# Optimization experiments

Hardware: AMD Instinct MI355X
Metric: run time of the kernel (lower is better)

## Reference

```python
import jax, jax.numpy as jnp
import numpy as np

B, T, C = 4, 2048, 1024
H = 16
D = C // H  # head_dim = 64


def setup_inputs() -> dict:
    key = jax.random.key(0)
    ks = jax.random.split(key, 9)
    s = 1.0 / np.sqrt(C)
    return {
        "x": jax.random.normal(ks[0], (B, T, C), dtype=jnp.float32),
        "Wk": jax.random.uniform(ks[1], (C, C), jnp.float32, -s, s),
        "bk": jax.random.uniform(ks[2], (C,), jnp.float32, -s, s),
        "Wq": jax.random.uniform(ks[3], (C, C), jnp.float32, -s, s),
        "bq": jax.random.uniform(ks[4], (C,), jnp.float32, -s, s),
        "Wv": jax.random.uniform(ks[5], (C, C), jnp.float32, -s, s),
        "bv": jax.random.uniform(ks[6], (C,), jnp.float32, -s, s),
        "Wp": jax.random.uniform(ks[7], (C, C), jnp.float32, -s, s),
        "bp": jax.random.uniform(ks[8], (C,), jnp.float32, -s, s),
    }


def reference(x, Wk, bk, Wq, bq, Wv, bv, Wp, bp):
    # projections -> (B, H, T, D)
    def split_heads(y):
        return y.reshape(B, T, H, D).transpose(0, 2, 1, 3)

    k = split_heads(x @ Wk.T + bk)
    q = split_heads(x @ Wq.T + bq)
    v = split_heads(x @ Wv.T + bv)

    att = jnp.einsum("bhtd,bhsd->bhts", q, k) / np.sqrt(D).astype(np.float32)
    causal = jnp.tril(jnp.ones((T, T), dtype=bool))
    att = jnp.where(causal, att, -jnp.inf)
    att = jax.nn.softmax(att, axis=-1)

    y = jnp.einsum("bhts,bhsd->bhtd", att, v)  # (B,H,T,D)
    y = y.transpose(0, 2, 1, 3).reshape(B, T, C)
    return y @ Wp.T + bp
```

## Files before the change

kernel.cpp:

```cpp
#include <hip/hip_runtime.h>
#include <hip/hip_bf16.h>

typedef unsigned short u16;
typedef unsigned int u32;
typedef short short8 __attribute__((ext_vector_type(8)));
typedef short short4v __attribute__((ext_vector_type(4)));
typedef float f32x4 __attribute__((ext_vector_type(4)));

#define MFMA16(a, b, c) __builtin_amdgcn_mfma_f32_16x16x32_bf16((a), (b), (c), 0, 0, 0)

constexpr int kB = 4, kT = 2048, kC = 1024, kH = 16, kD = 64;
constexpr int kBT = kB * kT;
constexpr long kQKV = (long)kB * kH * kT * kD;
constexpr float kSC = 0.125f * 1.4426950408889634f;

__device__ inline u16 f2bf(float f) {
    __hip_bfloat16 h = __float2bfloat16(f);
    return *reinterpret_cast<u16*>(&h);
}
__device__ inline u32 pkbf_trunc(float lo, float hi) {
    return __builtin_amdgcn_perm(__builtin_bit_cast(u32, hi),
                                 __builtin_bit_cast(u32, lo), 0x07060302u);
}
__device__ inline u32 pkbf_rne(float lo, float hi) {
    return ((u32)f2bf(hi) << 16) | (u32)f2bf(lo);
}

__device__ inline void cp16(const u16* g, u16* l) {
    __builtin_amdgcn_global_load_lds(
        (const __attribute__((address_space(1))) unsigned int*)g,
        (__attribute__((address_space(3))) unsigned int*)l, 16, 0, 0);
}

__global__ __launch_bounds__(256) void cast_kernel(
    const float* __restrict__ x,  const float* __restrict__ Wk,
    const float* __restrict__ Wq, const float* __restrict__ Wv,
    const float* __restrict__ Wp,
    u16* __restrict__ xb, u16* __restrict__ wkb, u16* __restrict__ wqb,
    u16* __restrict__ wvb, u16* __restrict__ wpb)
{
    const long id = (long)blockIdx.x * 256 + threadIdx.x;
    const float* src;
    u16* dst;
    long off;
    if (id < 2097152) {
        src = x; dst = xb; off = id;
    } else {
        const long w = (id - 2097152) >> 18;
        off = (id - 2097152) & 262143;
        src = (w == 0) ? Wk : (w == 1) ? Wq : (w == 2) ? Wv : Wp;
        dst = (w == 0) ? wkb : (w == 1) ? wqb : (w == 2) ? wvb : wpb;
    }
    f32x4 v = *(const f32x4*)&src[off * 4];
    short4v s = {(short)f2bf(v[0]), (short)f2bf(v[1]),
                 (short)f2bf(v[2]), (short)f2bf(v[3])};
    *(short4v*)&dst[off * 4] = s;
}


__global__ __launch_bounds__(512, 1) void qkv_gemm_bf16(
    const u16* __restrict__ xb, const u16* __restrict__ wall,
    const float* __restrict__ bk, const float* __restrict__ bq,
    const float* __restrict__ bv,
    u16* __restrict__ kw, u16* __restrict__ qw, u16* __restrict__ vw)
{
    __shared__ __align__(16) u16 A2[2][128 * 64];
    __shared__ __align__(16) u16 B2[2][256 * 64];

    const int tid = threadIdx.x;
    const int lane = tid & 63;
    const int wid = tid >> 6;
    const int l15 = lane & 15;
    const int quad = lane >> 4;
    const int wr = wid & 1;
    const int wc = wid >> 1;
    const int m0 = blockIdx.x * 128;
    const int n0c = blockIdx.y * 256;

    f32x4 zero = {0.f, 0.f, 0.f, 0.f};
    f32x4 acc[4][4];
#pragma unroll
    for (int i = 0; i < 4; ++i)
#pragma unroll
        for (int j = 0; j < 4; ++j) acc[i][j] = zero;

    const int vA = tid >> 3, chA = tid & 7;
    const int rowMa = ((vA >> 5) << 6) + (vA & 31);
    const int rowMb = rowMa + 32;
    const u16* aMaS = xb + (long)(m0 + rowMa) * kC + ((chA ^ (rowMa & 7)) * 8);
    const u16* aMbS = xb + (long)(m0 + rowMb) * kC + ((chA ^ (rowMb & 7)) * 8);
    const int aMaD = rowMa * 64 + chA * 8;
    const int aMbD = rowMb * 64 + chA * 8;
    const u16* bNaS[2]; const u16* bNbS[2];
    int bNaD[2], bNbD[2];
#pragma unroll
    for (int q = 0; q < 2; ++q) {
        const int slot = q * 512 + tid;
        const int v = slot >> 3, ch = slot & 7;
        const int ra = ((v >> 5) << 6) + (v & 31);
        const int rb = ra + 32;
        bNaS[q] = wall + (long)(n0c + ra) * kC + ((ch ^ (ra & 7)) * 8);
        bNbS[q] = wall + (long)(n0c + rb) * kC + ((ch ^ (rb & 7)) * 8);
        bNaD[q] = ra * 64 + ch * 8;
        bNbD[q] = rb * 64 + ch * 8;
    }

    int aOff[4][2], bOff[4][2];
#pragma unroll
    for (int i = 0; i < 4; ++i) {
        const int row = wr * 64 + i * 16 + l15;
#pragma unroll
        for (int k2 = 0; k2 < 2; ++k2)
            aOff[i][k2] = row * 64 + (((k2 * 4 + quad) ^ (row & 7)) * 8);
    }
#pragma unroll
    for (int j = 0; j < 4; ++j) {
        const int row = wc * 64 + j * 16 + l15;
#pragma unroll
        for (int k2 = 0; k2 < 2; ++k2)
            bOff[j][k2] = row * 64 + (((k2 * 4 + quad) ^ (row & 7)) * 8);
    }

    cp16(bNaS[0], &B2[0][bNaD[0]]);
    cp16(bNaS[1], &B2[0][bNaD[1]]);
    cp16(aMaS,    &A2[0][aMaD]);
    cp16(aMbS,    &A2[0][aMbD]);
    cp16(bNbS[0], &B2[0][bNbD[0]]);
    cp16(bNbS[1], &B2[0][bNbD[1]]);

#pragma unroll 2
    for (int t = 0; t < 16; ++t) {
        const int c = t & 1;
        const u16* Ab = A2[c];
        const u16* Bb = B2[c];
        u16* An = A2[c ^ 1];
        u16* Bn = B2[c ^ 1];
        const long ko = (long)(t + 1) * 64;
        const bool pf = (t < 15);

        short8 amL[2][2], amH[2][2], bnL[2][2], bnH[2][2];

        asm volatile("s_waitcnt vmcnt(2)" ::: "memory");
        __builtin_amdgcn_s_barrier();
        __builtin_amdgcn_sched_barrier(0);
#pragma unroll
        for (int i = 0; i < 2; ++i)
#pragma unroll
            for (int k2 = 0; k2 < 2; ++k2)
                amL[i][k2] = *(const short8*)&Ab[aOff[i][k2]];
#pragma unroll
        for (int j = 0; j < 2; ++j)
#pragma unroll
            for (int k2 = 0; k2 < 2; ++k2)
                bnL[j][k2] = *(const short8*)&Bb[bOff[j][k2]];
        if (pf) {
            cp16(bNaS[0] + ko, &Bn[bNaD[0]]);
            cp16(bNaS[1] + ko, &Bn[bNaD[1]]);
        }
        asm volatile("s_waitcnt lgkmcnt(0)" ::: "memory");
        __builtin_amdgcn_sched_barrier(0);
        __builtin_amdgcn_s_setprio(1);
#pragma unroll
        for (int i = 0; i < 2; ++i)
#pragma unroll
            for (int j = 0; j < 2; ++j) {
                acc[i][j] = MFMA16(amL[i][0], bnL[j][0], acc[i][j]);
                acc[i][j] = MFMA16(amL[i][1], bnL[j][1], acc[i][j]);
            }
        __builtin_amdgcn_s_setprio(0);

#pragma unroll
        for (int i = 0; i < 2; ++i)
#pragma unroll
            for (int k2 = 0; k2 < 2; ++k2)
                amH[i][k2] = *(const short8*)&Ab[aOff[2 + i][k2]];
        if (pf) {
            cp16(aMaS + ko, &An[aMaD]);
            cp16(aMbS + ko, &An[aMbD]);
        }
        asm volatile("s_waitcnt lgkmcnt(0)" ::: "memory");
        __builtin_amdgcn_sched_barrier(0);
        __builtin_amdgcn_s_setprio(1);
#pragma unroll
        for (int i = 0; i < 2; ++i)
#pragma unroll
            for (int j = 0; j < 2; ++j) {
                acc[2 + i][j] = MFMA16(amH[i][0], bnL[j][0], acc[2 + i][j]);
                acc[2 + i][j] = MFMA16(amH[i][1], bnL[j][1], acc[2 + i][j]);
            }
        __builtin_amdgcn_s_setprio(0);

        if (pf) {
            asm volatile("s_waitcnt vmcnt(4)" ::: "memory");
        } else {
            asm volatile("s_waitcnt vmcnt(0)" ::: "memory");
        }
        __builtin_amdgcn_s_barrier();
        __builtin_amdgcn_sched_barrier(0);
#pragma unroll
        for (int j = 0; j < 2; ++j)
#pragma unroll
            for (int k2 = 0; k2 < 2; ++k2)
                bnH[j][k2] = *(const short8*)&Bb[bOff[2 + j][k2]];
        if (pf) {
            cp16(bNbS[0] + ko, &Bn[bNbD[0]]);
            cp16(bNbS[1] + ko, &Bn[bNbD[1]]);
        }
        asm volatile("s_waitcnt lgkmcnt(0)" ::: "memory");
        __builtin_amdgcn_sched_barrier(0);
        __builtin_amdgcn_s_setprio(1);
#pragma unroll
        for (int i = 0; i < 2; ++i)
#pragma unroll
            for (int j = 0; j < 2; ++j) {
                acc[i][2 + j] = MFMA16(amL[i][0], bnH[j][0], acc[i][2 + j]);
                acc[i][2 + j] = MFMA16(amL[i][1], bnH[j][1], acc[i][2 + j]);
            }
        __builtin_amdgcn_s_setprio(0);

        __builtin_amdgcn_s_setprio(1);
#pragma unroll
        for (int i = 0; i < 2; ++i)
#pragma unroll
            for (int j = 0; j < 2; ++j) {
                acc[2 + i][2 + j] = MFMA16(amH[i][0], bnH[j][0], acc[2 + i][2 + j]);
                acc[2 + i][2 + j] = MFMA16(amH[i][1], bnH[j][1], acc[2 + i][2 + j]);
            }
        __builtin_amdgcn_s_setprio(0);
    }

    const int z = (n0c >> 10);
    const float scale = (z == 1) ? kSC : 1.0f;
    const float* bias = (z == 0) ? bk : (z == 1) ? bq : bv;
#pragma unroll
    for (int j = 0; j < 4; ++j) {
        const int n = n0c + wc * 64 + j * 16 + l15;
        const int np = n & 1023;
        const float bias_f = bias[np];
        const int h = np >> 6, d = np & 63;
#pragma unroll
        for (int i = 0; i < 4; ++i) {
#pragma unroll
            for (int r = 0; r < 4; ++r) {
                const int m = m0 + wr * 64 + i * 16 + quad * 4 + r;
                const int b = m >> 11, tt = m & 2047;
                const float v = (acc[i][j][r] + bias_f) * scale;
                const int bh = b * kH + h;
                if (z == 2) {
                    vw[((long)bh * kD + d) * kT + tt] = f2bf(v);
                } else {
                    u16* dst = (z == 0) ? kw : qw;
                    dst[((long)bh * kT + tt) * kD + d] = f2bf(v);
                }
            }
        }
    }
}

__global__ __launch_bounds__(256) void qkv_gemm_kernel(
    const float* __restrict__ x,
    const float* __restrict__ Wk, const float* __restrict__ bk,
    const float* __restrict__ Wq, const float* __restrict__ bq,
    const float* __restrict__ Wv, const float* __restrict__ bv,
    u16* __restrict__ kw, u16* __restrict__ qw, u16* __restrict__ vw)
{
    __shared__ u16 As[128 * 32];
    __shared__ u16 Bs[128 * 32];
    const int tid = threadIdx.x;
    const int lane = tid & 63;
    const int wid = tid >> 6;
    const int l15 = lane & 15;
    const int quad = lane >> 4;
    const int m0 = blockIdx.x * 128;
    const int n0 = blockIdx.y * 128;
    const int z = blockIdx.z;

    const float* W = (z == 0) ? Wk : (z == 1) ? Wq : Wv;
    const float* bias = (z == 0) ? bk : (z == 1) ? bq : bv;

    f32x4 zero = {0.f, 0.f, 0.f, 0.f};
    f32x4 acc[4][4];
#pragma unroll
    for (int i = 0; i < 4; ++i)
#pragma unroll
        for (int j = 0; j < 4; ++j) acc[i][j] = zero;

    const int wm = (wid & 1) * 64;
    const int wn = (wid >> 1) * 64;
    const int row4 = tid >> 3;
    const int col4 = (tid & 7) * 4;

    for (int k0 = 0; k0 < kC; k0 += 32) {
#pragma unroll
        for (int p = 0; p < 4; ++p) {
            const int r = p * 32 + row4;
            f32x4 xa = *(const f32x4*)&x[(long)(m0 + r) * kC + k0 + col4];
            f32x4 wa = *(const f32x4*)&W[(long)(n0 + r) * kC + k0 + col4];
            short4v xs = {(short)f2bf(xa[0]), (short)f2bf(xa[1]),
                          (short)f2bf(xa[2]), (short)f2bf(xa[3])};
            short4v wsv = {(short)f2bf(wa[0]), (short)f2bf(wa[1]),
                           (short)f2bf(wa[2]), (short)f2bf(wa[3])};
            *(short4v*)&As[r * 32 + col4] = xs;
            *(short4v*)&Bs[r * 32 + col4] = wsv;
        }
        __syncthreads();
        short8 af[4], bfr[4];
#pragma unroll
        for (int mt = 0; mt < 4; ++mt)
            af[mt] = *(const short8*)&As[(wm + mt * 16 + l15) * 32 + quad * 8];
#pragma unroll
        for (int nt = 0; nt < 4; ++nt)
            bfr[nt] = *(const short8*)&Bs[(wn + nt * 16 + l15) * 32 + quad * 8];
#pragma unroll
        for (int mt = 0; mt < 4; ++mt)
#pragma unroll
            for (int nt = 0; nt < 4; ++nt)
                acc[mt][nt] = MFMA16(af[mt], bfr[nt], acc[mt][nt]);
        __syncthreads();
    }

    const float scale = (z == 1) ? kSC : 1.0f;
#pragma unroll
    for (int nt = 0; nt < 4; ++nt) {
        const int n = n0 + wn + nt * 16 + l15;
        const float bias_f = bias[n];
        const int h = n >> 6, d = n & 63;
#pragma unroll
        for (int mt = 0; mt < 4; ++mt) {
#pragma unroll
            for (int r = 0; r < 4; ++r) {
                const int m = m0 + wm + mt * 16 + quad * 4 + r;
                const int b = m >> 11, t = m & 2047;
                const float v = (acc[mt][nt][r] + bias_f) * scale;
                const int bh = b * kH + h;
                if (z == 2) {
                    vw[((long)bh * kD + d) * kT + t] = f2bf(v);
                } else {
                    u16* dst = (z == 0) ? kw : qw;
                    dst[((long)bh * kT + t) * kD + d] = f2bf(v);
                }
            }
        }
    }
}

__global__ __launch_bounds__(128, 2) void attn_kernel(
    const u16* qw, const u16* kw, const u16* vw, u16* ow)
{
    __shared__ u16 Ks[2][64 * 64];
    __shared__ u16 VT[2][64 * 64];
    __shared__ u16 Pb[64 * 64];

    const int tid = threadIdx.x;
    const int lane = tid & 63;
    const int wid = tid >> 6;
    const int l15 = lane & 15;
    const int quad = lane >> 4;
    const int id = blockIdx.x;
    const int bh = id & 63;
    const int pr = id >> 6;

    const float NEG = -1.0e30f;
    f32x4 zero = {0.f, 0.f, 0.f, 0.f};
    const short8 onesf = {(short)0x3F80, (short)0x3F80, (short)0x3F80, (short)0x3F80,
                          (short)0x3F80, (short)0x3F80, (short)0x3F80, (short)0x3F80};

    const int rl7 = l15 & 7;

    const u16* kbase = kw + (long)bh * kT * kD;
    const u16* vbase = vw + (long)bh * kD * kT;

    const u16* kp[4];
    const u16* vp[4];
#pragma unroll
    for (int q = 0; q < 4; ++q) {
        const int slot = q * 128 + tid;
        const int row = slot >> 3;
        const int c = slot & 7;
        const int off = (c ^ (row & 7)) * 8;
        kp[q] = kbase + (long)row * kD + off;
        vp[q] = vbase + (long)row * kT + off;
    }

    auto stage = [&](int buf, int st) {
        u16* kd = Ks[buf];
        u16* vd = VT[buf];
#pragma unroll
        for (int q = 0; q < 4; ++q) {
            cp16(kp[q] + (long)st * (64 * kD), kd + (q * 128 + tid) * 8);
            cp16(vp[q] + st * 64,              vd + (q * 128 + tid) * 8);
        }
    };

#pragma unroll
    for (int ph = 0; ph < 2; ++ph) {
        const int qt64 = ph ? (31 - pr) : pr;
        const int tw = qt64 * 64 + wid * 32;
        const int n_st = qt64 + 1;

        __syncthreads();
        stage(0, 0);

        short8 qf[2][2];
#pragma unroll
        for (int g = 0; g < 2; ++g) {
            const u16* qp = qw + ((long)bh * kT + tw + g * 16 + l15) * kD;
            qf[g][0] = *(const short8*)&qp[quad * 8];
            qf[g][1] = *(const short8*)&qp[32 + quad * 8];
        }

        f32x4 oacc[4][2];
#pragma unroll
        for (int mo = 0; mo < 4; ++mo)
#pragma unroll
            for (int g = 0; g < 2; ++g) oacc[mo][g] = zero;
        f32x4 lsum[2] = {zero, zero};

        for (int st = 0; st < n_st; ++st) {
            __syncthreads();
            const int cur = st & 1;
            if (st + 1 < n_st) stage(cur ^ 1, st + 1);

            const u16* K_ = Ks[cur];
            const u16* V_ = VT[cur];

            f32x4 sacc[4][2];
            __builtin_amdgcn_s_setprio(1);
#pragma unroll
            for (int ms = 0; ms < 4; ++ms) {
                const int row = ms * 16 + l15;
                short8 kf0 = *(const short8*)&K_[row * 64 + ((quad ^ rl7) * 8)];
                short8 kf1 = *(const short8*)&K_[row * 64 + (((4 + quad) ^ rl7) * 8)];
#pragma unroll
                for (int g = 0; g < 2; ++g) {
                    sacc[ms][g] = MFMA16(kf0, qf[g][0], zero);
                    sacc[ms][g] = MFMA16(kf1, qf[g][1], sacc[ms][g]);
                }
            }
            __builtin_amdgcn_s_setprio(0);

            if (st == n_st - 1) {
#pragma unroll
                for (int g = 0; g < 2; ++g) {
                    const int tl = wid * 32 + g * 16 + l15;
#pragma unroll
                    for (int ms = 0; ms < 4; ++ms)
#pragma unroll
                        for (int r = 0; r < 4; ++r)
                            if (ms * 16 + quad * 4 + r > tl) sacc[ms][g][r] = NEG;
                }
            }

#pragma unroll
            for (int g = 0; g < 2; ++g) {
                const int prow = wid * 32 + g * 16 + l15;
#pragma unroll
                for (int ms = 0; ms < 4; ++ms) {
                    const float p0 = exp2f(sacc[ms][g][0]);
                    const float p1 = exp2f(sacc[ms][g][1]);
                    const float p2 = exp2f(sacc[ms][g][2]);
                    const float p3 = exp2f(sacc[ms][g][3]);
                    uint2 pk;
                    pk.x = pkbf_trunc(p0, p1);
                    pk.y = pkbf_trunc(p2, p3);
                    const int chunk = (ms * 2 + (quad >> 1)) ^ rl7;
                    *(uint2*)&Pb[prow * 64 + chunk * 8 + (quad & 1) * 4] = pk;
                }
            }

            short8 pf[2][2];
#pragma unroll
            for (int g = 0; g < 2; ++g) {
                const int prow = wid * 32 + g * 16 + l15;
                pf[g][0] = *(const short8*)&Pb[prow * 64 + ((quad ^ rl7) * 8)];
                pf[g][1] = *(const short8*)&Pb[prow * 64 + (((4 + quad) ^ rl7) * 8)];
                lsum[g] = MFMA16(onesf, pf[g][0], lsum[g]);
                lsum[g] = MFMA16(onesf, pf[g][1], lsum[g]);
            }

            __builtin_amdgcn_s_setprio(1);
#pragma unroll
            for (int mo = 0; mo < 4; ++mo) {
                const int row = mo * 16 + l15;
                short8 vf0 = *(const short8*)&V_[row * 64 + ((quad ^ rl7) * 8)];
                short8 vf1 = *(const short8*)&V_[row * 64 + (((4 + quad) ^ rl7) * 8)];
#pragma unroll
                for (int g = 0; g < 2; ++g) {
                    oacc[mo][g] = MFMA16(vf0, pf[g][0], oacc[mo][g]);
                    oacc[mo][g] = MFMA16(vf1, pf[g][1], oacc[mo][g]);
                }
            }
            __builtin_amdgcn_s_setprio(0);
        }

#pragma unroll
        for (int g = 0; g < 2; ++g) {
            const float inv = 1.0f / lsum[g][0];
            const int t = tw + g * 16 + l15;
            u16* op = ow + ((long)bh * kT + t) * kD;
#pragma unroll
            for (int mo = 0; mo < 4; ++mo) {
                uint2 ov;
                ov.x = pkbf_rne(oacc[mo][g][0] * inv, oacc[mo][g][1] * inv);
                ov.y = pkbf_rne(oacc[mo][g][2] * inv, oacc[mo][g][3] * inv);
                *(uint2*)&op[mo * 16 + quad * 4] = ov;
            }
        }
    }
}

__global__ __launch_bounds__(512, 1) void out_gemm_bf16(
    const u16* __restrict__ ob, const u16* __restrict__ wpb,
    const float* __restrict__ bp, float* __restrict__ out)
{
    __shared__ __align__(16) u16 A2[2][128 * 64];
    __shared__ __align__(16) u16 B2[2][256 * 64];

    const int tid = threadIdx.x;
    const int lane = tid & 63;
    const int wid = tid >> 6;
    const int l15 = lane & 15;
    const int quad = lane >> 4;
    const int wr = wid & 1;
    const int wc = wid >> 1;
    const int m0 = blockIdx.x * 128;
    const int n0 = blockIdx.y * 256;

    f32x4 zero = {0.f, 0.f, 0.f, 0.f};
    f32x4 acc[4][4];
#pragma unroll
    for (int i = 0; i < 4; ++i)
#pragma unroll
        for (int j = 0; j < 4; ++j) acc[i][j] = zero;

    const int vA = tid >> 3, chA = tid & 7;
    const int rowMa = ((vA >> 5) << 6) + (vA & 31);
    const int rowMb = rowMa + 32;
    const int mMa = m0 + rowMa, mMb = m0 + rowMb;
    const u16* aMaS = ob + (((long)(mMa >> 11) * kH) * kT + (mMa & 2047)) * kD
                      + ((chA ^ (rowMa & 7)) * 8);
    const u16* aMbS = ob + (((long)(mMb >> 11) * kH) * kT + (mMb & 2047)) * kD
                      + ((chA ^ (rowMb & 7)) * 8);
    const int aMaD = rowMa * 64 + chA * 8;
    const int aMbD = rowMb * 64 + chA * 8;

    const u16* bNaS[2]; const u16* bNbS[2];
    int bNaD[2], bNbD[2];
#pragma unroll
    for (int q = 0; q < 2; ++q) {
        const int slot = q * 512 + tid;
        const int v = slot >> 3, ch = slot & 7;
        const int ra = ((v >> 5) << 6) + (v & 31);
        const int rb = ra + 32;
        bNaS[q] = wpb + (long)(n0 + ra) * kC + ((ch ^ (ra & 7)) * 8);
        bNbS[q] = wpb + (long)(n0 + rb) * kC + ((ch ^ (rb & 7)) * 8);
        bNaD[q] = ra * 64 + ch * 8;
        bNbD[q] = rb * 64 + ch * 8;
    }

    int aOff[4][2], bOff[4][2];
#pragma unroll
    for (int i = 0; i < 4; ++i) {
        const int row = wr * 64 + i * 16 + l15;
#pragma unroll
        for (int k2 = 0; k2 < 2; ++k2)
            aOff[i][k2] = row * 64 + (((k2 * 4 + quad) ^ (row & 7)) * 8);
    }
#pragma unroll
    for (int j = 0; j < 4; ++j) {
        const int row = wc * 64 + j * 16 + l15;
#pragma unroll
        for (int k2 = 0; k2 < 2; ++k2)
            bOff[j][k2] = row * 64 + (((k2 * 4 + quad) ^ (row & 7)) * 8);
    }

    cp16(bNaS[0], &B2[0][bNaD[0]]);
    cp16(bNaS[1], &B2[0][bNaD[1]]);
    cp16(aMaS,    &A2[0][aMaD]);
    cp16(aMbS,    &A2[0][aMbD]);
    cp16(bNbS[0], &B2[0][bNbD[0]]);
    cp16(bNbS[1], &B2[0][bNbD[1]]);

#pragma unroll 2
    for (int t = 0; t < 16; ++t) {
        const int c = t & 1;
        const u16* Ab = A2[c];
        const u16* Bb = B2[c];
        u16* An = A2[c ^ 1];
        u16* Bn = B2[c ^ 1];
        const long koA = (long)(t + 1) * kT * kD;
        const long koB = (long)(t + 1) * 64;
        const bool pf = (t < 15);

        short8 amL[2][2], amH[2][2], bnL[2][2], bnH[2][2];

        asm volatile("s_waitcnt vmcnt(2)" ::: "memory");
        __builtin_amdgcn_s_barrier();
        __builtin_amdgcn_sched_barrier(0);
#pragma unroll
        for (int i = 0; i < 2; ++i)
#pragma unroll
            for (int k2 = 0; k2 < 2; ++k2)
                amL[i][k2] = *(const short8*)&Ab[aOff[i][k2]];
#pragma unroll
        for (int j = 0; j < 2; ++j)
#pragma unroll
            for (int k2 = 0; k2 < 2; ++k2)
                bnL[j][k2] = *(const short8*)&Bb[bOff[j][k2]];
        if (pf) {
            cp16(bNaS[0] + koB, &Bn[bNaD[0]]);
            cp16(bNaS[1] + koB, &Bn[bNaD[1]]);
        }
        asm volatile("s_waitcnt lgkmcnt(0)" ::: "memory");
        __builtin_amdgcn_sched_barrier(0);
        __builtin_amdgcn_s_setprio(1);
#pragma unroll
        for (int i = 0; i < 2; ++i)
#pragma unroll
            for (int j = 0; j < 2; ++j) {
                acc[i][j] = MFMA16(amL[i][0], bnL[j][0], acc[i][j]);
                acc[i][j] = MFMA16(amL[i][1], bnL[j][1], acc[i][j]);
            }
        __builtin_amdgcn_s_setprio(0);

#pragma unroll
        for (int i = 0; i < 2; ++i)
#pragma unroll
            for (int k2 = 0; k2 < 2; ++k2)
                amH[i][k2] = *(const short8*)&Ab[aOff[2 + i][k2]];
        if (pf) {
            cp16(aMaS + koA, &An[aMaD]);
            cp16(aMbS + koA, &An[aMbD]);
        }
        asm volatile("s_waitcnt lgkmcnt(0)" ::: "memory");
        __builtin_amdgcn_sched_barrier(0);
        __builtin_amdgcn_s_setprio(1);
#pragma unroll
        for (int i = 0; i < 2; ++i)
#pragma unroll
            for (int j = 0; j < 2; ++j) {
                acc[2 + i][j] = MFMA16(amH[i][0], bnL[j][0], acc[2 + i][j]);
                acc[2 + i][j] = MFMA16(amH[i][1], bnL[j][1], acc[2 + i][j]);
            }
        __builtin_amdgcn_s_setprio(0);

        if (pf) {
            asm volatile("s_waitcnt vmcnt(4)" ::: "memory");
        } else {
            asm volatile("s_waitcnt vmcnt(0)" ::: "memory");
        }
        __builtin_amdgcn_s_barrier();
        __builtin_amdgcn_sched_barrier(0);
#pragma unroll
        for (int j = 0; j < 2; ++j)
#pragma unroll
            for (int k2 = 0; k2 < 2; ++k2)
                bnH[j][k2] = *(const short8*)&Bb[bOff[2 + j][k2]];
        if (pf) {
            cp16(bNbS[0] + koB, &Bn[bNbD[0]]);
            cp16(bNbS[1] + koB, &Bn[bNbD[1]]);
        }
        asm volatile("s_waitcnt lgkmcnt(0)" ::: "memory");
        __builtin_amdgcn_sched_barrier(0);
        __builtin_amdgcn_s_setprio(1);
#pragma unroll
        for (int i = 0; i < 2; ++i)
#pragma unroll
            for (int j = 0; j < 2; ++j) {
                acc[i][2 + j] = MFMA16(amL[i][0], bnH[j][0], acc[i][2 + j]);
                acc[i][2 + j] = MFMA16(amL[i][1], bnH[j][1], acc[i][2 + j]);
            }
        __builtin_amdgcn_s_setprio(0);

        __builtin_amdgcn_s_setprio(1);
#pragma unroll
        for (int i = 0; i < 2; ++i)
#pragma unroll
            for (int j = 0; j < 2; ++j) {
                acc[2 + i][2 + j] = MFMA16(amH[i][0], bnH[j][0], acc[2 + i][2 + j]);
                acc[2 + i][2 + j] = MFMA16(amH[i][1], bnH[j][1], acc[2 + i][2 + j]);
            }
        __builtin_amdgcn_s_setprio(0);
    }

#pragma unroll
    for (int j = 0; j < 4; ++j) {
        const int n = n0 + wc * 64 + j * 16 + l15;
        const float bias_f = bp[n];
#pragma unroll
        for (int i = 0; i < 4; ++i) {
#pragma unroll
            for (int r = 0; r < 4; ++r) {
                const int m = m0 + wr * 64 + i * 16 + quad * 4 + r;
                out[(long)m * kC + n] = acc[i][j][r] + bias_f;
            }
        }
    }
}

__global__ __launch_bounds__(256) void out_gemm_kernel(
    const u16* __restrict__ ow, const float* __restrict__ Wp,
    const float* __restrict__ bp, float* __restrict__ out)
{
    __shared__ u16 As[128 * 32];
    __shared__ u16 Bs[128 * 32];
    const int tid = threadIdx.x;
    const int lane = tid & 63;
    const int wid = tid >> 6;
    const int l15 = lane & 15;
    const int quad = lane >> 4;
    const int m0 = blockIdx.x * 128;
    const int n0 = blockIdx.y * 128;

    f32x4 zero = {0.f, 0.f, 0.f, 0.f};
    f32x4 acc[4][4];
#pragma unroll
    for (int i = 0; i < 4; ++i)
#pragma unroll
        for (int j = 0; j < 4; ++j) acc[i][j] = zero;

    const int wm = (wid & 1) * 64;
    const int wn = (wid >> 1) * 64;

    const int r0 = tid >> 2;
    const int kkA = (tid & 3) * 8;
    const int r1 = r0 + 64;
    const int row4 = tid >> 3;
    const int col4 = (tid & 7) * 4;

    for (int k0 = 0; k0 < kC; k0 += 32) {
        {
            const int m = m0 + r0, b = m >> 11, t = m & 2047;
            const int kk = k0 + kkA, h = kk >> 6, d = kk & 63;
            *(short8*)&As[r0 * 32 + kkA] =
                *(const short8*)&ow[(((long)b * kH + h) * kT + t) * kD + d];
        }
        {
            const int m = m0 + r1, b = m >> 11, t = m & 2047;
            const int kk = k0 + kkA, h = kk >> 6, d = kk & 63;
            *(short8*)&As[r1 * 32 + kkA] =
                *(const short8*)&ow[(((long)b * kH + h) * kT + t) * kD + d];
        }
#pragma unroll
        for (int p = 0; p < 4; ++p) {
            const int r = p * 32 + row4;
            f32x4 wa = *(const f32x4*)&Wp[(long)(n0 + r) * kC + k0 + col4];
            short4v wsv = {(short)f2bf(wa[0]), (short)f2bf(wa[1]),
                           (short)f2bf(wa[2]), (short)f2bf(wa[3])};
            *(short4v*)&Bs[r * 32 + col4] = wsv;
        }
        __syncthreads();
        short8 af[4], bfr[4];
#pragma unroll
        for (int mt = 0; mt < 4; ++mt)
            af[mt] = *(const short8*)&As[(wm + mt * 16 + l15) * 32 + quad * 8];
#pragma unroll
        for (int nt = 0; nt < 4; ++nt)
            bfr[nt] = *(const short8*)&Bs[(wn + nt * 16 + l15) * 32 + quad * 8];
#pragma unroll
        for (int mt = 0; mt < 4; ++mt)
#pragma unroll
            for (int nt = 0; nt < 4; ++nt)
                acc[mt][nt] = MFMA16(af[mt], bfr[nt], acc[mt][nt]);
        __syncthreads();
    }

#pragma unroll
    for (int nt = 0; nt < 4; ++nt) {
        const int n = n0 + wn + nt * 16 + l15;
        const float bias_f = bp[n];
#pragma unroll
        for (int mt = 0; mt < 4; ++mt) {
#pragma unroll
            for (int r = 0; r < 4; ++r) {
                const int m = m0 + wm + mt * 16 + quad * 4 + r;
                out[(long)m * kC + n] = acc[mt][nt][r] + bias_f;
            }
        }
    }
}

extern "C" void kernel_launch(void* const* d_in, const int* in_sizes, int n_in,
                              void* d_out, int out_size, void* d_ws, size_t ws_size,
                              hipStream_t stream) {
    const float* x  = (const float*)d_in[0];
    const float* Wk = (const float*)d_in[1];
    const float* bk = (const float*)d_in[2];
    const float* Wq = (const float*)d_in[3];
    const float* bq = (const float*)d_in[4];
    const float* Wv = (const float*)d_in[5];
    const float* bv = (const float*)d_in[6];
    const float* Wp = (const float*)d_in[7];
    const float* bp = (const float*)d_in[8];
    float* out = (float*)d_out;

    u16* ws = (u16*)d_ws;
    const size_t kNeed = 72ull * 1024 * 1024;

    if (ws_size >= kNeed) {
        u16* k_ws = ws;
        u16* q_ws = ws + kQKV;
        u16* v_ws = ws + 2 * kQKV;
        u16* xb   = ws + 3 * kQKV;
        u16* o_ws = xb;
        u16* wkb  = ws + 4 * kQKV;
        u16* wqb  = wkb + (long)kC * kC;
        u16* wvb  = wqb + (long)kC * kC;
        u16* wpb  = wvb + (long)kC * kC;

        cast_kernel<<<12288, 256, 0, stream>>>(x, Wk, Wq, Wv, Wp,
                                               xb, wkb, wqb, wvb, wpb);
        qkv_gemm_bf16<<<dim3(kBT / 128, 12), 512, 0, stream>>>(
            xb, wkb, bk, bq, bv, k_ws, q_ws, v_ws);
        attn_kernel<<<1024, 128, 0, stream>>>(q_ws, k_ws, v_ws, o_ws);
        out_gemm_bf16<<<dim3(kBT / 128, kC / 256), 512, 0, stream>>>(
            o_ws, wpb, bp, out);
    } else {
        u16* k_ws = ws;
        u16* q_ws = ws + kQKV;
        u16* v_ws = ws + 2 * kQKV;
        u16* o_ws = q_ws;

        qkv_gemm_kernel<<<dim3(kBT / 128, kC / 128, 3), 256, 0, stream>>>(
            x, Wk, bk, Wq, bq, Wv, bv, k_ws, q_ws, v_ws);
        attn_kernel<<<1024, 128, 0, stream>>>(q_ws, k_ws, v_ws, o_ws);
        out_gemm_kernel<<<dim3(kBT / 128, kC / 128), 256, 0, stream>>>(
            o_ws, Wp, bp, out);
    }
}
```

Baseline: 257.0 us.

## Keep softmax probabilities in registers via permlane32 swap instead of LDS

Removes the shared-memory round trip for the P tile in attention. P is now packed to bf16 in registers and rearranged across lanes with permlane32_swap to match the MFMA B-operand layout. The V reads are permuted to the matching k ordering, using two 8-byte LDS loads instead of one 16-byte load. This drops the LDS store/load of P and the Pb buffer, which may help occupancy, but the V fragment loads become narrower.

```diff
diff --git a/kernel.cpp b/kernel.cpp
--- a/kernel.cpp
+++ b/kernel.cpp
@@ -6,6 +6,7 @@
 typedef short short8 __attribute__((ext_vector_type(8)));
 typedef short short4v __attribute__((ext_vector_type(4)));
 typedef float f32x4 __attribute__((ext_vector_type(4)));
+typedef unsigned int u32x4 __attribute__((ext_vector_type(4)));
 
 #define MFMA16(a, b, c) __builtin_amdgcn_mfma_f32_16x16x32_bf16((a), (b), (c), 0, 0, 0)
 
@@ -349,7 +350,6 @@
 {
     __shared__ u16 Ks[2][64 * 64];
     __shared__ u16 VT[2][64 * 64];
-    __shared__ u16 Pb[64 * 64];
 
     const int tid = threadIdx.x;
     const int lane = tid & 63;
@@ -451,43 +451,52 @@
                 }
             }
 
+            short8 pfr[2][2];
 #pragma unroll
             for (int g = 0; g < 2; ++g) {
-                const int prow = wid * 32 + g * 16 + l15;
-#pragma unroll
-                for (int ms = 0; ms < 4; ++ms) {
-                    const float p0 = exp2f(sacc[ms][g][0]);
-                    const float p1 = exp2f(sacc[ms][g][1]);
-                    const float p2 = exp2f(sacc[ms][g][2]);
-                    const float p3 = exp2f(sacc[ms][g][3]);
-                    uint2 pk;
-                    pk.x = pkbf_trunc(p0, p1);
-                    pk.y = pkbf_trunc(p2, p3);
-                    const int chunk = (ms * 2 + (quad >> 1)) ^ rl7;
-                    *(uint2*)&Pb[prow * 64 + chunk * 8 + (quad & 1) * 4] = pk;
+#pragma unroll
+                for (int k2 = 0; k2 < 2; ++k2) {
+                    const int msA = k2 * 2, msB = k2 * 2 + 1;
+                    const float a0 = exp2f(sacc[msA][g][0]);
+                    const float a1 = exp2f(sacc[msA][g][1]);
+                    const float a2 = exp2f(sacc[msA][g][2]);
+                    const float a3 = exp2f(sacc[msA][g][3]);
+                    const float b0 = exp2f(sacc[msB][g][0]);
+                    const float b1 = exp2f(sacc[msB][g][1]);
+                    const float b2 = exp2f(sacc[msB][g][2]);
+                    const float b3 = exp2f(sacc[msB][g][3]);
+                    const u32 LA = pkbf_trunc(a0, a1), HA = pkbf_trunc(a2, a3);
+                    const u32 LB = pkbf_trunc(b0, b1), HB = pkbf_trunc(b2, b3);
+                    auto pl = __builtin_amdgcn_permlane32_swap(LA, LB, false, false);
+                    auto phh = __builtin_amdgcn_permlane32_swap(HA, HB, false, false);
+                    u32x4 w;
+                    w[0] = pl[0]; w[1] = phh[0]; w[2] = pl[1]; w[3] = phh[1];
+                    pfr[g][k2] = __builtin_bit_cast(short8, w);
                 }
             }
 
-            short8 pf[2][2];
 #pragma unroll
             for (int g = 0; g < 2; ++g) {
-                const int prow = wid * 32 + g * 16 + l15;
-                pf[g][0] = *(const short8*)&Pb[prow * 64 + ((quad ^ rl7) * 8)];
-                pf[g][1] = *(const short8*)&Pb[prow * 64 + (((4 + quad) ^ rl7) * 8)];
-                lsum[g] = MFMA16(onesf, pf[g][0], lsum[g]);
-                lsum[g] = MFMA16(onesf, pf[g][1], lsum[g]);
+                lsum[g] = MFMA16(onesf, pfr[g][0], lsum[g]);
+                lsum[g] = MFMA16(onesf, pfr[g][1], lsum[g]);
             }
 
             __builtin_amdgcn_s_setprio(1);
 #pragma unroll
             for (int mo = 0; mo < 4; ++mo) {
                 const int row = mo * 16 + l15;
-                short8 vf0 = *(const short8*)&V_[row * 64 + ((quad ^ rl7) * 8)];
-                short8 vf1 = *(const short8*)&V_[row * 64 + (((4 + quad) ^ rl7) * 8)];
-#pragma unroll
-                for (int g = 0; g < 2; ++g) {
-                    oacc[mo][g] = MFMA16(vf0, pf[g][0], oacc[mo][g]);
-                    oacc[mo][g] = MFMA16(vf1, pf[g][1], oacc[mo][g]);
+#pragma unroll
+                for (int k2 = 0; k2 < 2; ++k2) {
+                    const int ch = k2 * 4 + (quad >> 1) * 2;
+                    const int hw = (quad & 1) * 4;
+                    uint2 v1 = *(const uint2*)&V_[row * 64 + ((ch ^ rl7) * 8) + hw];
+                    uint2 v2 = *(const uint2*)&V_[row * 64 + (((ch + 1) ^ rl7) * 8) + hw];
+                    u32x4 wv;
+                    wv[0] = v1.x; wv[1] = v1.y; wv[2] = v2.x; wv[3] = v2.y;
+                    const short8 vf = __builtin_bit_cast(short8, wv);
+#pragma unroll
+                    for (int g = 0; g < 2; ++g)
+                        oacc[mo][g] = MFMA16(vf, pfr[g][k2], oacc[mo][g]);
                 }
             }
             __builtin_amdgcn_s_setprio(0);
```

Result: slower. 272.2 us (+5.9%).

## Use 128-row query tiles with 4 waves and triple-buffered K/V staging

Applied to the files above, without the earlier changes.

The attention kernel moves from 64-row query tiles with 2 waves to 128-row tiles with 4 waves, so each staged K/V tile is shared by twice as many query rows. It also moves from double to triple buffering, using explicit vmcnt waits and raw barriers so loads run two stages ahead. The causal mask now covers the last two key tiles. This is meant to cut K/V global traffic per query and hide load latency, at the cost of more LDS per block and fewer blocks in the grid.

```diff
diff --git a/kernel.cpp b/kernel.cpp
--- a/kernel.cpp
+++ b/kernel.cpp
@@ -6,6 +6,7 @@
 typedef short short8 __attribute__((ext_vector_type(8)));
 typedef short short4v __attribute__((ext_vector_type(4)));
 typedef float f32x4 __attribute__((ext_vector_type(4)));
+typedef unsigned int u32x4 __attribute__((ext_vector_type(4)));
 
 #define MFMA16(a, b, c) __builtin_amdgcn_mfma_f32_16x16x32_bf16((a), (b), (c), 0, 0, 0)
 
@@ -344,12 +345,12 @@
     }
 }
 
-__global__ __launch_bounds__(128, 2) void attn_kernel(
+__global__ __launch_bounds__(256, 2) void attn_kernel(
     const u16* qw, const u16* kw, const u16* vw, u16* ow)
 {
-    __shared__ u16 Ks[2][64 * 64];
-    __shared__ u16 VT[2][64 * 64];
-    __shared__ u16 Pb[64 * 64];
+    __shared__ u16 Ks[3][64 * 64];
+    __shared__ u16 VT[3][64 * 64];
+    __shared__ u16 Pb[128 * 64];
 
     const int tid = threadIdx.x;
     const int lane = tid & 63;
@@ -358,7 +359,7 @@
     const int quad = lane >> 4;
     const int id = blockIdx.x;
     const int bh = id & 63;
-    const int pr = id >> 6;
+    const int pp = id >> 6;
 
     const float NEG = -1.0e30f;
     f32x4 zero = {0.f, 0.f, 0.f, 0.f};
@@ -370,36 +371,40 @@
     const u16* kbase = kw + (long)bh * kT * kD;
     const u16* vbase = vw + (long)bh * kD * kT;
 
-    const u16* kp[4];
-    const u16* vp[4];
-#pragma unroll
-    for (int q = 0; q < 4; ++q) {
-        const int slot = q * 128 + tid;
+    const u16* kp[2];
+    const u16* vp[2];
+    int sdst[2];
+#pragma unroll
+    for (int q = 0; q < 2; ++q) {
+        const int slot = q * 256 + tid;
         const int row = slot >> 3;
         const int c = slot & 7;
         const int off = (c ^ (row & 7)) * 8;
         kp[q] = kbase + (long)row * kD + off;
         vp[q] = vbase + (long)row * kT + off;
+        sdst[q] = slot * 8;
     }
 
     auto stage = [&](int buf, int st) {
         u16* kd = Ks[buf];
         u16* vd = VT[buf];
 #pragma unroll
-        for (int q = 0; q < 4; ++q) {
-            cp16(kp[q] + (long)st * (64 * kD), kd + (q * 128 + tid) * 8);
-            cp16(vp[q] + st * 64,              vd + (q * 128 + tid) * 8);
+        for (int q = 0; q < 2; ++q) {
+            cp16(kp[q] + (long)st * (64 * kD), kd + sdst[q]);
+            cp16(vp[q] + st * 64,              vd + sdst[q]);
         }
     };
 
 #pragma unroll
     for (int ph = 0; ph < 2; ++ph) {
-        const int qt64 = ph ? (31 - pr) : pr;
-        const int tw = qt64 * 64 + wid * 32;
-        const int n_st = qt64 + 1;
+        const int p = ph ? (15 - pp) : pp;
+        const int p2 = 2 * p;
+        const int n_st = p2 + 2;
+        const int tw = p * 128 + wid * 32;
 
         __syncthreads();
         stage(0, 0);
+        stage(1, 1);
 
         short8 qf[2][2];
 #pragma unroll
@@ -416,10 +421,21 @@
             for (int g = 0; g < 2; ++g) oacc[mo][g] = zero;
         f32x4 lsum[2] = {zero, zero};
 
+        int cur = 0;
         for (int st = 0; st < n_st; ++st) {
-            __syncthreads();
-            const int cur = st & 1;
-            if (st + 1 < n_st) stage(cur ^ 1, st + 1);
+            if (st + 1 < n_st) {
+                asm volatile("s_waitcnt vmcnt(4)" ::: "memory");
+            } else {
+                asm volatile("s_waitcnt vmcnt(0)" ::: "memory");
+            }
+            __builtin_amdgcn_s_barrier();
+            __builtin_amdgcn_sched_barrier(0);
+
+            const int nx2 = st + 2;
+            if (nx2 < n_st) {
+                const int nb = (cur + 2 >= 3) ? cur - 1 : cur + 2;
+                stage(nb, nx2);
+            }
 
             const u16* K_ = Ks[cur];
             const u16* V_ = VT[cur];
@@ -439,15 +455,16 @@
             }
             __builtin_amdgcn_s_setprio(0);
 
-            if (st == n_st - 1) {
+            const int dg = st - p2;
+            if (dg >= 0) {
 #pragma unroll
                 for (int g = 0; g < 2; ++g) {
-                    const int tl = wid * 32 + g * 16 + l15;
+                    const int off = wid * 32 + g * 16 + l15 - dg * 64;
 #pragma unroll
                     for (int ms = 0; ms < 4; ++ms)
 #pragma unroll
                         for (int r = 0; r < 4; ++r)
-                            if (ms * 16 + quad * 4 + r > tl) sacc[ms][g][r] = NEG;
+                            if (ms * 16 + quad * 4 + r > off) sacc[ms][g][r] = NEG;
                 }
             }
 
@@ -458,11 +475,11 @@
                 for (int ms = 0; ms < 4; ++ms) {
                     const float p0 = exp2f(sacc[ms][g][0]);
                     const float p1 = exp2f(sacc[ms][g][1]);
-                    const float p2 = exp2f(sacc[ms][g][2]);
+                    const float p2f = exp2f(sacc[ms][g][2]);
                     const float p3 = exp2f(sacc[ms][g][3]);
                     uint2 pk;
                     pk.x = pkbf_trunc(p0, p1);
-                    pk.y = pkbf_trunc(p2, p3);
+                    pk.y = pkbf_trunc(p2f, p3);
                     const int chunk = (ms * 2 + (quad >> 1)) ^ rl7;
                     *(uint2*)&Pb[prow * 64 + chunk * 8 + (quad & 1) * 4] = pk;
                 }
@@ -491,6 +508,8 @@
                 }
             }
             __builtin_amdgcn_s_setprio(0);
+
+            cur = (cur == 2) ? 0 : cur + 1;
         }
 
 #pragma unroll
@@ -812,7 +831,7 @@
                                                xb, wkb, wqb, wvb, wpb);
         qkv_gemm_bf16<<<dim3(kBT / 128, 12), 512, 0, stream>>>(
             xb, wkb, bk, bq, bv, k_ws, q_ws, v_ws);
-        attn_kernel<<<1024, 128, 0, stream>>>(q_ws, k_ws, v_ws, o_ws);
+        attn_kernel<<<512, 256, 0, stream>>>(q_ws, k_ws, v_ws, o_ws);
         out_gemm_bf16<<<dim3(kBT / 128, kC / 256), 512, 0, stream>>>(
             o_ws, wpb, bp, out);
     } else {
@@ -823,7 +842,7 @@
 
         qkv_gemm_kernel<<<dim3(kBT / 128, kC / 128, 3), 256, 0, stream>>>(
             x, Wk, bk, Wq, bq, Wv, bv, k_ws, q_ws, v_ws);
-        attn_kernel<<<1024, 128, 0, stream>>>(q_ws, k_ws, v_ws, o_ws);
+        attn_kernel<<<512, 256, 0, stream>>>(q_ws, k_ws, v_ws, o_ws);
         out_gemm_kernel<<<dim3(kBT / 128, kC / 128), 256, 0, stream>>>(
             o_ws, Wp, bp, out);
     }
```

After: 260.1 us. No clear change (+1.2%).
